# Kernel optimization log

Measured on AMD Instinct MI355X. Metric: run time of the kernel, lower is better.

## Reference

```python
import jax, jax.numpy as jnp
import numpy as np

N = 50000        # nodes
E = 800000       # edges (avg degree 16)
F = 64           # num_features
G = 128          # number of graphs in the batch
NOUT = 1         # n_output


def setup_inputs() -> dict:
    key = jax.random.key(0)
    ks = jax.random.split(key, 9)
    x = jax.random.normal(ks[0], (N, F), dtype=jnp.float32)
    edge_index = jax.random.randint(ks[1], (2, E), 0, N, dtype=jnp.int64)
    batch = jnp.sort(jax.random.randint(ks[2], (N,), 0, G, dtype=jnp.int64))
    W1 = jax.random.normal(ks[3], (F, F), dtype=jnp.float32) * 0.1
    b1 = jnp.zeros((F,), dtype=jnp.float32)
    W2 = jax.random.normal(ks[4], (F, 2 * F), dtype=jnp.float32) * 0.1
    b2 = jnp.zeros((2 * F,), dtype=jnp.float32)
    fcW = jax.random.normal(ks[5], (2 * F, NOUT), dtype=jnp.float32) * 0.1
    fcb = jnp.zeros((NOUT,), dtype=jnp.float32)
    return {"x": x, "edge_index": edge_index, "batch": batch,
            "W1": W1, "b1": b1, "W2": W2, "b2": b2, "fcW": fcW, "fcb": fcb}


def reference(x, edge_index, batch, W1, b1, W2, b2, fcW, fcb):
    n = x.shape[0]
    # PyG GCNConv: add self-loops, symmetric normalization D^-1/2 (A+I) D^-1/2
    loop = jnp.arange(n, dtype=edge_index.dtype)
    src = jnp.concatenate([edge_index[0], loop])  # [E+N]
    dst = jnp.concatenate([edge_index[1], loop])  # [E+N]
    deg = jax.ops.segment_sum(jnp.ones_like(dst, dtype=x.dtype), dst, num_segments=n)
    dinv = jnp.where(deg > 0, jax.lax.rsqrt(jnp.maximum(deg, 1.0)), 0.0)
    norm = dinv[src] * dinv[dst]                  # [E+N]

    def gcn_conv(h, W, b):
        h = h @ W                                 # [N, Fout]
        msg = h[src] * norm[:, None]              # gather + scale, [E+N, Fout]
        return jax.ops.segment_sum(msg, dst, num_segments=n) + b

    h1 = jax.nn.relu(gcn_conv(x, W1, b1))         # [N, F]
    h2 = jax.nn.relu(gcn_conv(h1, W2, b2))        # [N, 2F]

    # global mean pool per graph (dropout is identity in eval)
    counts = jax.ops.segment_sum(jnp.ones((n,), x.dtype), batch, num_segments=G)
    pooled = jax.ops.segment_sum(h2, batch, num_segments=G)
    pooled = pooled / jnp.maximum(counts, 1.0)[:, None]  # [G, 2F]

    out = pooled @ fcW + fcb                      # [G, NOUT]
    return out.reshape(1, -1)                     # [1, G*NOUT]
```

## Files before the change

kernel.cpp:

```cpp
#include <hip/hip_runtime.h>
#include <hip/hip_bf16.h>

typedef __hip_bfloat16 bf16;

static __device__ __forceinline__ float loadF(const void* p, long long i, int f32){
  return f32 ? ((const float*)p)[i] : __bfloat162float(((const bf16*)p)[i]);
}
static __device__ __forceinline__ int loadI(const void* p, long long i, int i64){
  return i64 ? (int)((const long long*)p)[i] : ((const int*)p)[i];
}
static __device__ __forceinline__ unsigned short f2bf(float f){
  unsigned u = __float_as_uint(f);
  return (unsigned short)((u + 0x7FFFu + ((u>>16)&1u)) >> 16);
}
static __device__ __forceinline__ float bf2f(unsigned v){
  return __uint_as_float(v<<16);
}

#define CAP 4096
#define LB_EDGES 4096

__global__ void k_init(const unsigned int* __restrict__ xw, const unsigned int* __restrict__ eiw,
                       int* __restrict__ flags, int* __restrict__ gcursor, int nbuckets,
                       float* __restrict__ S, int gn){
  int i = blockIdx.x*256 + threadIdx.x;
  if(i < nbuckets) gcursor[i] = 0;
  if(i < gn) S[i] = 0.f;
  if(blockIdx.x == 0){
    __shared__ int s1, s2;
    if(threadIdx.x==0){ s1=0; s2=0; }
    __syncthreads();
    unsigned w = xw[threadIdx.x];
    int e = (int)((w>>7)&0xFFu);
    if(e>=110 && e<=135) atomicAdd(&s1, 1);
    if(eiw[2*threadIdx.x+1] != 0u) atomicAdd(&s2, 1);
    __syncthreads();
    if(threadIdx.x==0){
      flags[0] = (s1 < 128) ? 1 : 0;
      flags[1] = (s2 < 128) ? 1 : 0;
    }
  }
}

__global__ __launch_bounds__(256) void k_logbuild(const void* __restrict__ ei, int E, int N,
                                                  const int* __restrict__ flags,
                                                  int* __restrict__ gcursor,
                                                  unsigned int* __restrict__ log, int nbuckets){
  __shared__ unsigned int stash[LB_EDGES];
  __shared__ int hcnt[1024];
  __shared__ int hbase[1024];
  int t = threadIdx.x;
  for(int b=t; b<nbuckets; b+=256) hcnt[b] = 0;
  __syncthreads();
  int i64 = flags[1];
  long long e0 = (long long)blockIdx.x*LB_EDGES;
  int cnt = (int)(((long long)E - e0) < LB_EDGES ? ((long long)E - e0) : LB_EDGES);
  for(int k=t; k<cnt; k+=256){
    long long e = e0 + k;
    int s = loadI(ei, e, i64);                 s = min(max(s,0), N-1);
    int d = loadI(ei, (long long)E + e, i64);  d = min(max(d,0), N-1);
    unsigned p = (((unsigned)d)<<16) | (unsigned)s;
    stash[k] = p;
    atomicAdd(&hcnt[d>>6], 1);
  }
  __syncthreads();
  for(int b=t; b<nbuckets; b+=256){
    int c = hcnt[b];
    hbase[b] = (c>0) ? atomicAdd(&gcursor[b], c) : 0;
    hcnt[b] = 0;
  }
  __syncthreads();
  for(int k=t; k<cnt; k+=256){
    unsigned p = stash[k];
    int b = (int)(p>>22);
    int pos = hbase[b] + atomicAdd(&hcnt[b], 1);
    if(pos < CAP) log[(long long)b*CAP + pos] = p;
  }
}

__global__ __launch_bounds__(256) void k_bsortg0(const unsigned int* __restrict__ log,
                                                 const int* __restrict__ gcursor,
                                                 unsigned short* __restrict__ csr,
                                                 int* __restrict__ beg, int* __restrict__ endv,
                                                 float* __restrict__ dinv,
                                                 const void* __restrict__ x, const int* __restrict__ flags,
                                                 unsigned short* __restrict__ g0, int N){
  __shared__ int hist[64];
  __shared__ int cur[64];
  __shared__ float dloc[64];
  int b = blockIdx.x, t = threadIdx.x;
  if(t < 64) hist[t] = 0;
  __syncthreads();
  int n = min(gcursor[b], CAP);
  const unsigned int* L = log + (long long)b*CAP;
  for(int j=t; j<n; j+=256) atomicAdd(&hist[(L[j]>>16)&63], 1);
  __syncthreads();
  if(t < 64){
    int v = hist[t];
    int inc = v;
    #pragma unroll
    for(int o=1; o<64; o<<=1){
      int u = __shfl_up(inc, o);
      if(t >= o) inc += u;
    }
    int excl = inc - v;
    cur[t] = excl;
    float dv = rsqrtf((float)(v + 1));
    dloc[t] = dv;
    int node = b*64 + t;
    if(node < N){
      int base = b*CAP + excl;
      beg[node]  = base;
      endv[node] = base + v;
      dinv[node] = dv;
    }
  }
  __syncthreads();
  unsigned short* C = csr + (long long)b*CAP;
  for(int j=t; j<n; j+=256){
    unsigned p = L[j];
    int l = (int)((p>>16)&63u);
    int pos = atomicAdd(&cur[l], 1);
    C[pos] = (unsigned short)(p & 0xFFFFu);
  }
  int f32 = flags[0];
  long long base = (long long)b*64*64;
  for(int i=t; i<4096; i+=256){
    int nl = i>>6;
    int node = b*64 + nl;
    if(node < N) g0[base + i] = f2bf(loadF(x, base + i, f32) * dloc[nl]);
  }
}

__global__ __launch_bounds__(256) void k_agg(const unsigned short* __restrict__ g,
                                             const unsigned short* __restrict__ csr,
                                             const int* __restrict__ beg, const int* __restrict__ endv,
                                             const float* __restrict__ dinv,
                                             unsigned int* __restrict__ out32, int N){
  int node = blockIdx.x*4 + (threadIdx.x>>6);
  int lane = threadIdx.x&63;
  if(node >= N) return;
  int half = lane>>5, fl = lane&31;
  const unsigned int* G32 = (const unsigned int*)g;
  int j = beg[node], e = endv[node];
  float2 a0={0.f,0.f}, a1={0.f,0.f}, a2={0.f,0.f}, a3={0.f,0.f};
  float2 a4={0.f,0.f}, a5={0.f,0.f}, a6={0.f,0.f}, a7={0.f,0.f};
  for(; j+16<=e; j+=16){
    int s0 = csr[j +  0 + half];
    int s1 = csr[j +  2 + half];
    int s2 = csr[j +  4 + half];
    int s3 = csr[j +  6 + half];
    int s4 = csr[j +  8 + half];
    int s5 = csr[j + 10 + half];
    int s6 = csr[j + 12 + half];
    int s7 = csr[j + 14 + half];
    unsigned v0 = G32[(long long)s0*32 + fl];
    unsigned v1 = G32[(long long)s1*32 + fl];
    unsigned v2 = G32[(long long)s2*32 + fl];
    unsigned v3 = G32[(long long)s3*32 + fl];
    unsigned v4 = G32[(long long)s4*32 + fl];
    unsigned v5 = G32[(long long)s5*32 + fl];
    unsigned v6 = G32[(long long)s6*32 + fl];
    unsigned v7 = G32[(long long)s7*32 + fl];
    a0.x += bf2f(v0 & 0xFFFFu); a0.y += bf2f(v0 >> 16);
    a1.x += bf2f(v1 & 0xFFFFu); a1.y += bf2f(v1 >> 16);
    a2.x += bf2f(v2 & 0xFFFFu); a2.y += bf2f(v2 >> 16);
    a3.x += bf2f(v3 & 0xFFFFu); a3.y += bf2f(v3 >> 16);
    a4.x += bf2f(v4 & 0xFFFFu); a4.y += bf2f(v4 >> 16);
    a5.x += bf2f(v5 & 0xFFFFu); a5.y += bf2f(v5 >> 16);
    a6.x += bf2f(v6 & 0xFFFFu); a6.y += bf2f(v6 >> 16);
    a7.x += bf2f(v7 & 0xFFFFu); a7.y += bf2f(v7 >> 16);
  }
  for(; j+8<=e; j+=8){
    int s0 = csr[j + 0 + half];
    int s1 = csr[j + 2 + half];
    int s2 = csr[j + 4 + half];
    int s3 = csr[j + 6 + half];
    unsigned v0 = G32[(long long)s0*32 + fl];
    unsigned v1 = G32[(long long)s1*32 + fl];
    unsigned v2 = G32[(long long)s2*32 + fl];
    unsigned v3 = G32[(long long)s3*32 + fl];
    a0.x += bf2f(v0 & 0xFFFFu); a0.y += bf2f(v0 >> 16);
    a1.x += bf2f(v1 & 0xFFFFu); a1.y += bf2f(v1 >> 16);
    a2.x += bf2f(v2 & 0xFFFFu); a2.y += bf2f(v2 >> 16);
    a3.x += bf2f(v3 & 0xFFFFu); a3.y += bf2f(v3 >> 16);
  }
  for(; j+2<=e; j+=2){
    int s = csr[j + half];
    unsigned v = G32[(long long)s*32 + fl];
    a0.x += bf2f(v & 0xFFFFu); a0.y += bf2f(v >> 16);
  }
  if(j < e && half == 0){
    int s = csr[j];
    unsigned v = G32[(long long)s*32 + fl];
    a0.x += bf2f(v & 0xFFFFu); a0.y += bf2f(v >> 16);
  }
  float sx = ((a0.x+a1.x)+(a2.x+a3.x)) + ((a4.x+a5.x)+(a6.x+a7.x));
  float sy = ((a0.y+a1.y)+(a2.y+a3.y)) + ((a4.y+a5.y)+(a6.y+a7.y));
  sx += __shfl_xor(sx, 32, 64);
  sy += __shfl_xor(sy, 32, 64);
  unsigned sv = G32[(long long)node*32 + fl];
  float dv = dinv[node];
  sx = (sx + bf2f(sv & 0xFFFFu)) * dv;
  sy = (sy + bf2f(sv >> 16)) * dv;
  if(half == 0)
    out32[(long long)node*32 + fl] = (unsigned)f2bf(sx) | ((unsigned)f2bf(sy) << 16);
}

__global__ __launch_bounds__(256) void k_gemm1(const unsigned int* __restrict__ A32, const void* __restrict__ W,
                                               const void* __restrict__ b, const int* __restrict__ flags,
                                               const float* __restrict__ dinv, unsigned short* __restrict__ out, int N){
  __shared__ float Ws[64*64];
  __shared__ float xs[128*65];
  int f32 = flags[0];
  int tid = threadIdx.x;
  for(int i=tid;i<4096;i+=256) Ws[i] = loadF(W, i, f32);
  int row0 = blockIdx.x*128;
  for(int i=tid;i<4096;i+=256){
    int r = i>>5, kd = i&31;
    int gr = row0 + r;
    unsigned v = (gr<N) ? A32[(long long)gr*32 + kd] : 0u;
    xs[r*65 + 2*kd    ] = bf2f(v & 0xFFFFu);
    xs[r*65 + 2*kd + 1] = bf2f(v >> 16);
  }
  __syncthreads();
  int cg = tid&15, rg = tid>>4;
  int col_g = cg*4, row_g = rg*8;
  float acc[8][4];
  #pragma unroll
  for(int r=0;r<8;r++){ acc[r][0]=0.f; acc[r][1]=0.f; acc[r][2]=0.f; acc[r][3]=0.f; }
  for(int k=0;k<64;k++){
    float4 w = *(const float4*)&Ws[k*64 + col_g];
    float xr[8];
    #pragma unroll
    for(int r=0;r<8;r++) xr[r] = xs[(row_g+r)*65 + k];
    #pragma unroll
    for(int r=0;r<8;r++){
      acc[r][0] += xr[r]*w.x; acc[r][1] += xr[r]*w.y;
      acc[r][2] += xr[r]*w.z; acc[r][3] += xr[r]*w.w;
    }
  }
  float b0 = loadF(b, col_g,   f32), b1v = loadF(b, col_g+1, f32);
  float b2v = loadF(b, col_g+2, f32), b3 = loadF(b, col_g+3, f32);
  #pragma unroll
  for(int r=0;r<8;r++){
    int gr = row0 + row_g + r;
    if(gr<N){
      float dv = dinv[gr];
      float v0 = acc[r][0]+b0, v1 = acc[r][1]+b1v, v2 = acc[r][2]+b2v, v3 = acc[r][3]+b3;
      v0 = (v0>0.f?v0:0.f)*dv; v1 = (v1>0.f?v1:0.f)*dv;
      v2 = (v2>0.f?v2:0.f)*dv; v3 = (v3>0.f?v3:0.f)*dv;
      ushort4 st;
      st.x = f2bf(v0); st.y = f2bf(v1); st.z = f2bf(v2); st.w = f2bf(v3);
      *(ushort4*)&out[(long long)gr*64 + col_g] = st;
    }
  }
}

__global__ __launch_bounds__(256) void k_gemm2pool(const unsigned int* __restrict__ A32, const void* __restrict__ W,
                                                   const void* __restrict__ b, const void* __restrict__ fcW,
                                                   const void* __restrict__ batch, const int* __restrict__ flags,
                                                   float* __restrict__ S, int N, int NOUT){
  __shared__ float Ws[64*128];
  __shared__ float xs[128*65];
  __shared__ float Sloc[128*4];
  __shared__ int gid[128];
  int f32 = flags[0], i64 = flags[1];
  int tid = threadIdx.x;
  int row0 = blockIdx.x*128;
  for(int i=tid;i<8192;i+=256) Ws[i] = loadF(W, i, f32);
  for(int i=tid;i<4096;i+=256){
    int r = i>>5, kd = i&31;
    int gr = row0 + r;
    unsigned v = (gr<N) ? A32[(long long)gr*32 + kd] : 0u;
    xs[r*65 + 2*kd    ] = bf2f(v & 0xFFFFu);
    xs[r*65 + 2*kd + 1] = bf2f(v >> 16);
  }
  if(tid < 128){
    int node = row0 + tid;
    gid[tid] = (node < N) ? loadI(batch, node, i64) : 0;
  }
  for(int i=tid;i<512;i+=256) Sloc[i] = 0.f;
  __syncthreads();
  int cg = tid&15, rg = tid>>4;
  int c0 = cg*4, c1 = 64 + cg*4, row_g = rg*8;
  float acc[8][8];
  #pragma unroll
  for(int r=0;r<8;r++)
    #pragma unroll
    for(int c=0;c<8;c++) acc[r][c]=0.f;
  for(int k=0;k<64;k++){
    float4 w0 = *(const float4*)&Ws[k*128 + c0];
    float4 w1 = *(const float4*)&Ws[k*128 + c1];
    float xr[8];
    #pragma unroll
    for(int r=0;r<8;r++) xr[r] = xs[(row_g+r)*65 + k];
    #pragma unroll
    for(int r=0;r<8;r++){
      acc[r][0] += xr[r]*w0.x; acc[r][1] += xr[r]*w0.y;
      acc[r][2] += xr[r]*w0.z; acc[r][3] += xr[r]*w0.w;
      acc[r][4] += xr[r]*w1.x; acc[r][5] += xr[r]*w1.y;
      acc[r][6] += xr[r]*w1.z; acc[r][7] += xr[r]*w1.w;
    }
  }
  #pragma unroll
  for(int c=0;c<8;c++){
    int col = (c<4) ? (c0+c) : (c1+c-4);
    float bb = loadF(b, col, f32);
    #pragma unroll
    for(int r=0;r<8;r++){ float z = acc[r][c]+bb; acc[r][c] = z>0.f?z:0.f; }
  }
  int nv = N - row0; nv = nv < 128 ? nv : 128;
  if(nv <= 0) return;
  int gmin = gid[0], gmax = gid[nv-1];
  bool ldsOK = (NOUT <= 4) && (gmax - gmin < 128);
  for(int o=0;o<NOUT;o++){
    float fw[8];
    #pragma unroll
    for(int c=0;c<8;c++){
      int col = (c<4) ? (c0+c) : (c1+c-4);
      fw[c] = loadF(fcW, (long long)col*NOUT + o, f32);
    }
    #pragma unroll
    for(int r=0;r<8;r++){
      float z = acc[r][0]*fw[0] + acc[r][1]*fw[1] + acc[r][2]*fw[2] + acc[r][3]*fw[3]
              + acc[r][4]*fw[4] + acc[r][5]*fw[5] + acc[r][6]*fw[6] + acc[r][7]*fw[7];
      #pragma unroll
      for(int m=1;m<16;m<<=1) z += __shfl_xor(z, m, 64);
      int nl = row_g + r;
      if(cg==0 && nl < nv){
        int gg = gid[nl];
        if(ldsOK) atomicAdd(&Sloc[(gg-gmin)*NOUT + o], z);
        else      atomicAdd(&S[(long long)gg*NOUT + o], z);
      }
    }
  }
  if(ldsOK){
    __syncthreads();
    int nbin = (gmax - gmin + 1)*NOUT;
    for(int i=tid; i<nbin; i+=256){
      float v = Sloc[i];
      if(v != 0.f){
        int bin = i / NOUT, o = i - bin*NOUT;
        atomicAdd(&S[(long long)(gmin+bin)*NOUT + o], v);
      }
    }
  }
}

static __device__ __forceinline__ int lower_bound_batch(const void* batch, int N, int key, int i64){
  int lo = 0, hi = N;
  while(lo < hi){ int mid = (lo+hi)>>1; if(loadI(batch, mid, i64) < key) lo = mid+1; else hi = mid; }
  return lo;
}

__global__ void k_final2(const float* __restrict__ S, const void* __restrict__ batch, int N,
                         const int* __restrict__ flags, const void* __restrict__ fcb,
                         void* __restrict__ out, int G, int NOUT){
  int f32 = flags[0], i64 = flags[1];
  int g = blockIdx.x*256 + threadIdx.x;
  if(g >= G) return;
  int c = lower_bound_batch(batch, N, g+1, i64) - lower_bound_batch(batch, N, g, i64);
  float inv = 1.f / (float)(c > 0 ? c : 1);
  for(int o=0;o<NOUT;o++){
    float r = S[(long long)g*NOUT+o]*inv + loadF(fcb, o, f32);
    if(f32) ((float*)out)[g*NOUT+o] = r;
    else    ((unsigned short*)out)[g*NOUT+o] = f2bf(r);
  }
}

extern "C" void kernel_launch(void* const* d_in, const int* in_sizes, int n_in,
                              void* d_out, int out_size, void* d_ws, size_t ws_size,
                              hipStream_t stream) {
  const void* x    = d_in[0];
  const void* ei   = d_in[1];
  const void* batch= d_in[2];
  const void* W1   = d_in[3];
  const void* b1   = d_in[4];
  const void* W2   = d_in[5];
  const void* b2   = d_in[6];
  const void* fcW  = d_in[7];
  const void* fcb  = d_in[8];

  const int N = in_sizes[0] / 64;
  const int E = in_sizes[1] / 2;
  const int NOUT = in_sizes[8];
  const int G = out_size / NOUT;
  const int nbuckets = (N + 63) >> 6;

  size_t off = 0;
  auto alloc = [&](size_t bytes) -> char* {
    char* p = (char*)d_ws + off;
    off += (bytes + 511) & ~(size_t)511;
    return p;
  };
  int*   flags   = (int*)  alloc(512);
  int*   gcursor = (int*)  alloc((size_t)nbuckets*4);
  float* dinv    = (float*)alloc((size_t)N*4);
  int*   beg     = (int*)  alloc((size_t)N*4);
  int*   endv    = (int*)  alloc((size_t)N*4);
  float* S       = (float*)alloc((size_t)G*NOUT*4);
  unsigned int*   log  = (unsigned int*)  alloc((size_t)nbuckets*CAP*4);
  unsigned short* csr  = (unsigned short*)alloc((size_t)nbuckets*CAP*2);
  unsigned short* g0   = (unsigned short*)alloc((size_t)N*64*2);
  unsigned short* g1   = (unsigned short*)alloc((size_t)N*64*2);
  unsigned int*   aBuf = (unsigned int*)  alloc((size_t)N*32*4);
  (void)ws_size; (void)n_in;

  int initgrid = (nbuckets > G*NOUT ? nbuckets : G*NOUT);

  k_init    <<<(initgrid+255)/256, 256, 0, stream>>>((const unsigned int*)x, (const unsigned int*)ei,
                                                     flags, gcursor, nbuckets, S, G*NOUT);
  k_logbuild<<<(E+LB_EDGES-1)/LB_EDGES, 256, 0, stream>>>(ei, E, N, flags, gcursor, log, nbuckets);
  k_bsortg0 <<<nbuckets,      256, 0, stream>>>(log, gcursor, csr, beg, endv, dinv, x, flags, g0, N);

  k_agg     <<<(N+3)/4,       256, 0, stream>>>(g0, csr, beg, endv, dinv, aBuf, N);
  k_gemm1   <<<(N+127)/128,   256, 0, stream>>>(aBuf, W1, b1, flags, dinv, g1, N);
  k_agg     <<<(N+3)/4,       256, 0, stream>>>(g1, csr, beg, endv, dinv, aBuf, N);
  k_gemm2pool<<<(N+127)/128,  256, 0, stream>>>(aBuf, W2, b2, fcW, batch, flags, S, N, NOUT);

  k_final2  <<<(G+255)/256,   256, 0, stream>>>(S, batch, N, flags, fcb, d_out, G, NOUT);
}
```

Measured before the change: 213.4 us.

## Apply W1 before aggregation and fuse it into the edge-log build launch

```diff
diff --git a/kernel.cpp b/kernel.cpp
--- a/kernel.cpp
+++ b/kernel.cpp
@@ -18,7 +18,7 @@
 }
 
 #define CAP 4096
-#define LB_EDGES 4096
+#define LB_EDGES 2048
 
 __global__ void k_init(const unsigned int* __restrict__ xw, const unsigned int* __restrict__ eiw,
                        int* __restrict__ flags, int* __restrict__ gcursor, int nbuckets,
@@ -42,39 +42,82 @@
   }
 }
 
-__global__ __launch_bounds__(256) void k_logbuild(const void* __restrict__ ei, int E, int N,
-                                                  const int* __restrict__ flags,
-                                                  int* __restrict__ gcursor,
-                                                  unsigned int* __restrict__ log, int nbuckets){
-  __shared__ unsigned int stash[LB_EDGES];
-  __shared__ int hcnt[1024];
-  __shared__ int hbase[1024];
+__global__ __launch_bounds__(256) void k_pre(const void* __restrict__ ei, int E, int N,
+                                             const int* __restrict__ flags,
+                                             int* __restrict__ gcursor,
+                                             unsigned int* __restrict__ log, int nbuckets,
+                                             const void* __restrict__ x, const void* __restrict__ W,
+                                             unsigned short* __restrict__ y, int nLog){
+  __shared__ unsigned int smem[12416];
   int t = threadIdx.x;
-  for(int b=t; b<nbuckets; b+=256) hcnt[b] = 0;
-  __syncthreads();
-  int i64 = flags[1];
-  long long e0 = (long long)blockIdx.x*LB_EDGES;
-  int cnt = (int)(((long long)E - e0) < LB_EDGES ? ((long long)E - e0) : LB_EDGES);
-  for(int k=t; k<cnt; k+=256){
-    long long e = e0 + k;
-    int s = loadI(ei, e, i64);                 s = min(max(s,0), N-1);
-    int d = loadI(ei, (long long)E + e, i64);  d = min(max(d,0), N-1);
-    unsigned p = (((unsigned)d)<<16) | (unsigned)s;
-    stash[k] = p;
-    atomicAdd(&hcnt[d>>6], 1);
-  }
-  __syncthreads();
-  for(int b=t; b<nbuckets; b+=256){
-    int c = hcnt[b];
-    hbase[b] = (c>0) ? atomicAdd(&gcursor[b], c) : 0;
-    hcnt[b] = 0;
-  }
-  __syncthreads();
-  for(int k=t; k<cnt; k+=256){
-    unsigned p = stash[k];
-    int b = (int)(p>>22);
-    int pos = hbase[b] + atomicAdd(&hcnt[b], 1);
-    if(pos < CAP) log[(long long)b*CAP + pos] = p;
+  if((int)blockIdx.x < nLog){
+    unsigned int* stash = smem;
+    int* hcnt  = (int*)(smem + LB_EDGES);
+    int* hbase = (int*)(smem + LB_EDGES + 1024);
+    for(int b=t; b<nbuckets; b+=256) hcnt[b] = 0;
+    __syncthreads();
+    int i64 = flags[1];
+    long long e0 = (long long)blockIdx.x*LB_EDGES;
+    int cnt = (int)(((long long)E - e0) < LB_EDGES ? ((long long)E - e0) : LB_EDGES);
+    for(int k=t; k<cnt; k+=256){
+      long long e = e0 + k;
+      int s = loadI(ei, e, i64);                 s = min(max(s,0), N-1);
+      int d = loadI(ei, (long long)E + e, i64);  d = min(max(d,0), N-1);
+      unsigned p = (((unsigned)d)<<16) | (unsigned)s;
+      stash[k] = p;
+      atomicAdd(&hcnt[d>>6], 1);
+    }
+    __syncthreads();
+    for(int b=t; b<nbuckets; b+=256){
+      int c = hcnt[b];
+      hbase[b] = (c>0) ? atomicAdd(&gcursor[b], c) : 0;
+      hcnt[b] = 0;
+    }
+    __syncthreads();
+    for(int k=t; k<cnt; k+=256){
+      unsigned p = stash[k];
+      int b = (int)(p>>22);
+      int pos = hbase[b] + atomicAdd(&hcnt[b], 1);
+      if(pos < CAP) log[(long long)b*CAP + pos] = p;
+    }
+  } else {
+    float* Ws = (float*)smem;
+    float* xs = (float*)(smem + 4096);
+    int f32 = flags[0];
+    for(int i=t;i<4096;i+=256) Ws[i] = loadF(W, i, f32);
+    int row0 = ((int)blockIdx.x - nLog)*128;
+    for(int i=t;i<8192;i+=256){
+      int r = i>>6, c = i&63;
+      int gr = row0 + r;
+      xs[r*65 + c] = (gr<N) ? loadF(x, (long long)gr*64 + c, f32) : 0.f;
+    }
+    __syncthreads();
+    int cg = t&15, rg = t>>4;
+    int col_g = cg*4, row_g = rg*8;
+    float acc[8][4];
+    #pragma unroll
+    for(int r=0;r<8;r++){ acc[r][0]=0.f; acc[r][1]=0.f; acc[r][2]=0.f; acc[r][3]=0.f; }
+    for(int k=0;k<64;k++){
+      float4 w = *(const float4*)&Ws[k*64 + col_g];
+      float xr[8];
+      #pragma unroll
+      for(int r=0;r<8;r++) xr[r] = xs[(row_g+r)*65 + k];
+      #pragma unroll
+      for(int r=0;r<8;r++){
+        acc[r][0] += xr[r]*w.x; acc[r][1] += xr[r]*w.y;
+        acc[r][2] += xr[r]*w.z; acc[r][3] += xr[r]*w.w;
+      }
+    }
+    #pragma unroll
+    for(int r=0;r<8;r++){
+      int gr = row0 + row_g + r;
+      if(gr<N){
+        ushort4 st;
+        st.x = f2bf(acc[r][0]); st.y = f2bf(acc[r][1]);
+        st.z = f2bf(acc[r][2]); st.w = f2bf(acc[r][3]);
+        *(ushort4*)&y[(long long)gr*64 + col_g] = st;
+      }
+    }
   }
 }
 
@@ -83,8 +126,8 @@
                                                  unsigned short* __restrict__ csr,
                                                  int* __restrict__ beg, int* __restrict__ endv,
                                                  float* __restrict__ dinv,
-                                                 const void* __restrict__ x, const int* __restrict__ flags,
-                                                 unsigned short* __restrict__ g0, int N){
+                                                 const unsigned int* __restrict__ Y32,
+                                                 unsigned int* __restrict__ G032, int N){
   __shared__ int hist[64];
   __shared__ int cur[64];
   __shared__ float dloc[64];
@@ -123,12 +166,16 @@
     int pos = atomicAdd(&cur[l], 1);
     C[pos] = (unsigned short)(p & 0xFFFFu);
   }
-  int f32 = flags[0];
-  long long base = (long long)b*64*64;
-  for(int i=t; i<4096; i+=256){
-    int nl = i>>6;
+  long long base32 = (long long)b*2048;
+  for(int i=t; i<2048; i+=256){
+    int nl = i>>5;
     int node = b*64 + nl;
-    if(node < N) g0[base + i] = f2bf(loadF(x, base + i, f32) * dloc[nl]);
+    if(node < N){
+      unsigned v = Y32[base32 + i];
+      float dv = dloc[nl];
+      G032[base32 + i] = (unsigned)f2bf(bf2f(v & 0xFFFFu)*dv)
+                       | ((unsigned)f2bf(bf2f(v >> 16)*dv) << 16);
+    }
   }
 }
 
@@ -136,6 +183,8 @@
                                              const unsigned short* __restrict__ csr,
                                              const int* __restrict__ beg, const int* __restrict__ endv,
                                              const float* __restrict__ dinv,
+                                             const void* __restrict__ bias, const int* __restrict__ flags,
+                                             int mode,
                                              unsigned int* __restrict__ out32, int N){
   int node = blockIdx.x*4 + (threadIdx.x>>6);
   int lane = threadIdx.x&63;
@@ -203,58 +252,15 @@
   float dv = dinv[node];
   sx = (sx + bf2f(sv & 0xFFFFu)) * dv;
   sy = (sy + bf2f(sv >> 16)) * dv;
+  if(mode){
+    int f32 = flags[0];
+    float bx = loadF(bias, 2*fl,   f32);
+    float by = loadF(bias, 2*fl+1, f32);
+    sx = fmaxf(sx + bx, 0.f) * dv;
+    sy = fmaxf(sy + by, 0.f) * dv;
+  }
   if(half == 0)
     out32[(long long)node*32 + fl] = (unsigned)f2bf(sx) | ((unsigned)f2bf(sy) << 16);
-}
-
-__global__ __launch_bounds__(256) void k_gemm1(const unsigned int* __restrict__ A32, const void* __restrict__ W,
-                                               const void* __restrict__ b, const int* __restrict__ flags,
-                                               const float* __restrict__ dinv, unsigned short* __restrict__ out, int N){
-  __shared__ float Ws[64*64];
-  __shared__ float xs[128*65];
-  int f32 = flags[0];
-  int tid = threadIdx.x;
-  for(int i=tid;i<4096;i+=256) Ws[i] = loadF(W, i, f32);
-  int row0 = blockIdx.x*128;
-  for(int i=tid;i<4096;i+=256){
-    int r = i>>5, kd = i&31;
-    int gr = row0 + r;
-    unsigned v = (gr<N) ? A32[(long long)gr*32 + kd] : 0u;
-    xs[r*65 + 2*kd    ] = bf2f(v & 0xFFFFu);
-    xs[r*65 + 2*kd + 1] = bf2f(v >> 16);
-  }
-  __syncthreads();
-  int cg = tid&15, rg = tid>>4;
-  int col_g = cg*4, row_g = rg*8;
-  float acc[8][4];
-  #pragma unroll
-  for(int r=0;r<8;r++){ acc[r][0]=0.f; acc[r][1]=0.f; acc[r][2]=0.f; acc[r][3]=0.f; }
-  for(int k=0;k<64;k++){
-    float4 w = *(const float4*)&Ws[k*64 + col_g];
-    float xr[8];
-    #pragma unroll
-    for(int r=0;r<8;r++) xr[r] = xs[(row_g+r)*65 + k];
-    #pragma unroll
-    for(int r=0;r<8;r++){
-      acc[r][0] += xr[r]*w.x; acc[r][1] += xr[r]*w.y;
-      acc[r][2] += xr[r]*w.z; acc[r][3] += xr[r]*w.w;
-    }
-  }
-  float b0 = loadF(b, col_g,   f32), b1v = loadF(b, col_g+1, f32);
-  float b2v = loadF(b, col_g+2, f32), b3 = loadF(b, col_g+3, f32);
-  #pragma unroll
-  for(int r=0;r<8;r++){
-    int gr = row0 + row_g + r;
-    if(gr<N){
-      float dv = dinv[gr];
-      float v0 = acc[r][0]+b0, v1 = acc[r][1]+b1v, v2 = acc[r][2]+b2v, v3 = acc[r][3]+b3;
-      v0 = (v0>0.f?v0:0.f)*dv; v1 = (v1>0.f?v1:0.f)*dv;
-      v2 = (v2>0.f?v2:0.f)*dv; v3 = (v3>0.f?v3:0.f)*dv;
-      ushort4 st;
-      st.x = f2bf(v0); st.y = f2bf(v1); st.z = f2bf(v2); st.w = f2bf(v3);
-      *(ushort4*)&out[(long long)gr*64 + col_g] = st;
-    }
-  }
 }
 
 __global__ __launch_bounds__(256) void k_gemm2pool(const unsigned int* __restrict__ A32, const void* __restrict__ W,
@@ -402,21 +408,27 @@
   float* S       = (float*)alloc((size_t)G*NOUT*4);
   unsigned int*   log  = (unsigned int*)  alloc((size_t)nbuckets*CAP*4);
   unsigned short* csr  = (unsigned short*)alloc((size_t)nbuckets*CAP*2);
+  unsigned short* yB   = (unsigned short*)alloc((size_t)N*64*2);
   unsigned short* g0   = (unsigned short*)alloc((size_t)N*64*2);
   unsigned short* g1   = (unsigned short*)alloc((size_t)N*64*2);
   unsigned int*   aBuf = (unsigned int*)  alloc((size_t)N*32*4);
   (void)ws_size; (void)n_in;
 
   int initgrid = (nbuckets > G*NOUT ? nbuckets : G*NOUT);
+  int nLog = (E + LB_EDGES - 1) / LB_EDGES;
+  int nGem = (N + 127) / 128;
 
   k_init    <<<(initgrid+255)/256, 256, 0, stream>>>((const unsigned int*)x, (const unsigned int*)ei,
                                                      flags, gcursor, nbuckets, S, G*NOUT);
-  k_logbuild<<<(E+LB_EDGES-1)/LB_EDGES, 256, 0, stream>>>(ei, E, N, flags, gcursor, log, nbuckets);
-  k_bsortg0 <<<nbuckets,      256, 0, stream>>>(log, gcursor, csr, beg, endv, dinv, x, flags, g0, N);
-
-  k_agg     <<<(N+3)/4,       256, 0, stream>>>(g0, csr, beg, endv, dinv, aBuf, N);
-  k_gemm1   <<<(N+127)/128,   256, 0, stream>>>(aBuf, W1, b1, flags, dinv, g1, N);
-  k_agg     <<<(N+3)/4,       256, 0, stream>>>(g1, csr, beg, endv, dinv, aBuf, N);
+  k_pre     <<<nLog + nGem,   256, 0, stream>>>(ei, E, N, flags, gcursor, log, nbuckets,
+                                                x, W1, yB, nLog);
+  k_bsortg0 <<<nbuckets,      256, 0, stream>>>(log, gcursor, csr, beg, endv, dinv,
+                                                (const unsigned int*)yB, (unsigned int*)g0, N);
+
+  k_agg     <<<(N+3)/4,       256, 0, stream>>>(g0, csr, beg, endv, dinv, b1, flags, 1,
+                                                (unsigned int*)g1, N);
+  k_agg     <<<(N+3)/4,       256, 0, stream>>>(g1, csr, beg, endv, dinv, b1, flags, 0,
+                                                aBuf, N);
   k_gemm2pool<<<(N+127)/128,  256, 0, stream>>>(aBuf, W2, b2, fcW, batch, flags, S, N, NOUT);
 
   k_final2  <<<(G+255)/256,   256, 0, stream>>>(S, batch, N, flags, fcb, d_out, G, NOUT);
```

Result: no change. 212.1 us (-0.6%).
